# Performance work log

Measured on AMD Instinct MI355X. Metric: run time of the kernel, lower is better.

The kernel has to match this reference:

```python
import jax, jax.numpy as jnp
import numpy as np

B, L, N_APPS, EMB_DIM = 4096, 1024, 10, 2


def _linear_init(key, fan_in, fan_out):
    k1, k2 = jax.random.split(key)
    s = 1.0 / np.sqrt(fan_in)
    W = jax.random.uniform(k1, (fan_in, fan_out), minval=-s, maxval=s, dtype=jnp.float32)
    b = jax.random.uniform(k2, (fan_out,), minval=-s, maxval=s, dtype=jnp.float32)
    return W, b


def setup_inputs() -> dict:
    key = jax.random.key(0)
    ks = jax.random.split(key, 12)
    # features: row 0 carries integer-valued app ids (cast with .long() in torch)
    app_row = jax.random.randint(ks[0], (B, 1, L), 0, N_APPS).astype(jnp.float32)
    loads = jax.random.normal(ks[1], (B, 2, L), dtype=jnp.float32)
    features = jnp.concatenate([app_row, loads], axis=1)  # [B,3,L]
    x_app = jax.random.randint(ks[2], (B, 1), 0, N_APPS).astype(jnp.float32)
    x_load = jax.random.normal(ks[3], (B, 2), dtype=jnp.float32)
    x_features = jnp.concatenate([x_app, x_load], axis=1)  # [B,3]
    lengths = jax.random.randint(ks[4], (B,), 1, L + 1)  # dead in the math (see notes)
    emb = jax.random.normal(ks[5], (N_APPS, EMB_DIM), dtype=jnp.float32)
    fW1, fb1 = _linear_init(ks[6], EMB_DIM + 2, 50)
    fW2, fb2 = _linear_init(ks[7], 50, 25)
    fW3, fb3 = _linear_init(ks[8], 25, 5)
    rW1, rb1 = _linear_init(ks[9], 2 * 5 + EMB_DIM + 2, 50)
    rW2, rb2 = _linear_init(ks[10], 50, 25)
    rW3, rb3 = _linear_init(ks[11], 25, 1)
    return dict(x_features=x_features, features=features, lengths=lengths, emb=emb,
                fW1=fW1, fb1=fb1, fW2=fW2, fb2=fb2, fW3=fW3, fb3=fb3,
                rW1=rW1, rb1=rb1, rW2=rW2, rb2=rb2, rW3=rW3, rb3=rb3)


def _embed(table, idx):
    # nn.Embedding(max_norm=1.0): rows are renormalized to norm <= 1 at lookup
    e = table[idx]
    n = jnp.sqrt(jnp.sum(e * e, axis=-1, keepdims=True))
    return e * jnp.minimum(1.0, 1.0 / jnp.maximum(n, 1e-7))


def _mlp3(x, W1, b1, W2, b2, W3, b3):
    h = jax.nn.relu(x @ W1 + b1)
    h = jax.nn.relu(h @ W2 + b2)
    return h @ W3 + b3


def reference(x_features, features, lengths, emb,
              fW1, fb1, fW2, fb2, fW3, fb3,
              rW1, rb1, rW2, rb2, rW3, rb3):
    # NOTE: the torch forward slices xf[:, :xl] but then overwrites it with the
    # full-length rows, so `lengths` does not affect the math. Reproduced here.
    app_ids = features[:, 0, :].astype(jnp.int32)            # [B,L]
    loads = jnp.transpose(features[:, 1:, :], (0, 2, 1))     # [B,L,2]
    e = _embed(emb, app_ids)                                  # [B,L,2]
    h = jnp.concatenate([e, loads], axis=-1)                  # [B,L,4]
    h = _mlp3(h, fW1, fb1, fW2, fb2, fW3, fb3)                # [B,L,5]
    h_sum = jnp.sum(h, axis=1)                                # [B,5]
    h_max = jnp.max(h, axis=1)                                # [B,5]
    x_app = _embed(emb, x_features[:, 0].astype(jnp.int32))   # [B,2]
    x_f = jnp.concatenate([x_app, x_features[:, 1:]], axis=-1)  # [B,4]
    hh = jnp.concatenate([h_sum, h_max, x_f], axis=-1)        # [B,14]
    return _mlp3(hh, rW1, rb1, rW2, rb2, rW3, rb3)            # [B,1]
```

## Files before the change

### kernel.cpp

```cpp
#include <hip/hip_runtime.h>
#include <stdint.h>

#define BSZ 4096
#define LSEQ 1024

typedef _Float16 half8 __attribute__((ext_vector_type(8)));
typedef __fp16 fp16x2 __attribute__((ext_vector_type(2)));
typedef float f32x4 __attribute__((ext_vector_type(4)));

union S8 { int i[4]; half8 h; int4 q; };

__device__ __forceinline__ int pack_f16(float a, float b) {
    union { _Float16 h[2]; int i; } u;
    u.h[0] = (_Float16)a;
    u.h[1] = (_Float16)b;
    return u.i;
}
__device__ __forceinline__ int relu_pkrtz(float a, float b) {
    fp16x2 h = __builtin_amdgcn_cvt_pkrtz(a, b);
    h = __builtin_elementwise_max(h, (fp16x2)0.f);
    union { fp16x2 v; int i; } u;
    u.v = h;
    return u.i;
}
__device__ __forceinline__ void split_pair_f16(float a, float b, int& dh, int& dl) {
    _Float16 ah = (_Float16)a, bh = (_Float16)b;
    float al = a - (float)ah, bl = b - (float)bh;
    union { _Float16 h[2]; int i; } uh, ul;
    uh.h[0] = ah; uh.h[1] = bh;
    ul.h[0] = (_Float16)al; ul.h[1] = (_Float16)bl;
    dh = uh.i; dl = ul.i;
}
__device__ __forceinline__ f32x4 MFMA(half8 a, half8 b, f32x4 c) {
    return __builtin_amdgcn_mfma_f32_16x16x32_f16(a, b, c, 0, 0, 0);
}

#define WS_EMBH 5376
#define WS_EMBL 5392
#define WS_EMBR 5408

__global__ void sp_prep(const float* __restrict__ emb,
                        const float* __restrict__ fW1, const float* __restrict__ fb1,
                        const float* __restrict__ fW2, const float* __restrict__ fb2,
                        const float* __restrict__ fW3, const float* __restrict__ fb3,
                        int* __restrict__ ws)
{
    const int lane = threadIdx.x;
    const int L = lane & 15, g = lane >> 4;
    int4* wf = (int4*)ws;

    #pragma unroll
    for (int mt = 0; mt < 4; ++mt) {
        int j1 = ((mt >> 1) << 5) + ((L >> 2) << 3) + ((mt & 1) << 2) + (L & 3);
        float wv[4];
        _Float16 ah[4]; float alv[4];
        #pragma unroll
        for (int c = 0; c < 4; ++c) {
            wv[c] = (j1 < 50) ? fW1[c * 50 + j1] : 0.f;
            ah[c] = (_Float16)wv[c];
            alv[c] = wv[c] - (float)ah[c];
        }
        float bb = (j1 < 50) ? fb1[j1] : (j1 == 63 ? 1.f : 0.f);
        _Float16 bh = (_Float16)bb;
        float blv = bb - (float)bh;
        _Float16 v[8];
        #pragma unroll
        for (int e = 0; e < 8; ++e) {
            _Float16 x = (_Float16)0.f;
            if (g == 0) {
                if (e < 4) x = ah[e];
                else if (e < 6) x = ah[e - 4];
                else if (e == 6) x = bh;
            } else if (g == 1) {
                if (e < 4) x = (_Float16)alv[e];
                else if (e < 6) x = (_Float16)alv[e - 4];
                else if (e == 6) x = (_Float16)blv;
            }
            v[e] = x;
        }
        S8 F;
        #pragma unroll
        for (int d = 0; d < 4; ++d) {
            union { _Float16 h[2]; int i; } u;
            u.h[0] = v[2 * d]; u.h[1] = v[2 * d + 1];
            F.i[d] = u.i;
        }
        wf[mt * 64 + lane] = F.q;
    }

    #pragma unroll
    for (int kt = 0; kt < 2; ++kt) {
        #pragma unroll
        for (int mt2 = 0; mt2 < 2; ++mt2) {
            int j2 = ((L >> 2) << 3) + (mt2 << 2) + (L & 3);
            float w[8];
            #pragma unroll
            for (int r = 0; r < 8; ++r) {
                int j1v = kt * 32 + 8 * g + r;
                float wv = 0.f;
                if (j1v < 50)       wv = (j2 < 25) ? fW2[j1v * 25 + j2] : 0.f;
                else if (j1v == 63) wv = (j2 < 25) ? fb2[j2] : (j2 == 31 ? 1.f : 0.f);
                w[r] = wv;
            }
            S8 H, Lo;
            #pragma unroll
            for (int d = 0; d < 4; ++d) split_pair_f16(w[2*d], w[2*d+1], H.i[d], Lo.i[d]);
            wf[(4 + kt * 2 + mt2) * 64 + lane] = H.q;
            wf[(8 + kt * 2 + mt2) * 64 + lane] = Lo.q;
        }
    }

    {
        int m = L;
        float w[8];
        #pragma unroll
        for (int r = 0; r < 8; ++r) {
            int j2v = 8 * g + r;
            float wv = 0.f;
            if (j2v < 25)       wv = (m < 5) ? fW3[j2v * 5 + m] : 0.f;
            else if (j2v == 31) wv = (m < 5) ? fb3[m] : 0.f;
            w[r] = wv;
        }
        S8 H, Lo;
        #pragma unroll
        for (int d = 0; d < 4; ++d) split_pair_f16(w[2*d], w[2*d+1], H.i[d], Lo.i[d]);
        wf[12 * 64 + lane] = H.q;
        wf[13 * 64 + lane] = Lo.q;
    }

    if (lane < 10) {
        float a0 = emb[2 * lane], a1 = emb[2 * lane + 1];
        float n = sqrtf(a0 * a0 + a1 * a1);
        float s = fminf(1.f, 1.f / fmaxf(n, 1e-7f));
        float e0 = a0 * s, e1 = a1 * s;
        int dh, dl;
        split_pair_f16(e0, e1, dh, dl);
        ws[WS_EMBH + lane] = dh;
        ws[WS_EMBL + lane] = dl;
        ((float*)ws)[WS_EMBR + 2 * lane] = e0;
        ((float*)ws)[WS_EMBR + 2 * lane + 1] = e1;
    }
}

__global__ __launch_bounds__(256, 4) void sp_main(
    const float* __restrict__ x_features,
    const float* __restrict__ features,
    const int* __restrict__ ws,
    const float* __restrict__ rW1, const float* __restrict__ rb1,
    const float* __restrict__ rW2, const float* __restrict__ rb2,
    const float* __restrict__ rW3, const float* __restrict__ rb3,
    float* __restrict__ out)
{
    __shared__ int2 embhl[16];
    __shared__ float embr[20];
    __shared__ int4 bseq[LSEQ + 4];
    __shared__ float redS[4][5], redM[4][5];
    __shared__ float hhs[14];
    __shared__ float r1buf[50];

    const int t = threadIdx.x;
    const int b = blockIdx.x;
    const int lane = t & 63;
    const int wid = t >> 6;
    const int L = lane & 15;

    const int4* wf = (const int4*)ws;
    S8 A1[4], A2H[4], A2L[4], A3H, A3L;
    #pragma unroll
    for (int f = 0; f < 4; ++f)  A1[f].q  = wf[f * 64 + lane];
    #pragma unroll
    for (int f = 0; f < 4; ++f)  A2H[f].q = wf[(4 + f) * 64 + lane];
    #pragma unroll
    for (int f = 0; f < 4; ++f)  A2L[f].q = wf[(8 + f) * 64 + lane];
    A3H.q = wf[12 * 64 + lane];
    A3L.q = wf[13 * 64 + lane];

    if (t < 16) { embhl[t] = make_int2(ws[WS_EMBH + t], ws[WS_EMBL + t]); }
    if (t < 20) embr[t] = ((const float*)ws)[WS_EMBR + t];
    __syncthreads();

    const float* f0 = features + (size_t)b * (3 * LSEQ);
    #pragma unroll
    for (int j = 0; j < 4; ++j) {
        const int p = t + 256 * j;
        float av = f0[p];
        float bv = f0[LSEQ + p];
        float cv = f0[2 * LSEQ + p];
        int2 e = embhl[(int)av];
        bseq[p + j] = make_int4(e.x, pack_f16(bv, cv), e.y, 0x00003C00);
    }
    __syncthreads();

    float rs[4] = {0.f, 0.f, 0.f, 0.f};
    float rm[4] = {-3.4e38f, -3.4e38f, -3.4e38f, -3.4e38f};
    const f32x4 kzero = {0.f, 0.f, 0.f, 0.f};

    const int lbase = wid * 257 + L;

    #pragma unroll 2
    for (int it = 0; it < 8; ++it) {
        S8 B1a, B1b;
        B1a.q = bseq[lbase + it * 16];
        B1b.q = bseq[lbase + (it + 8) * 16];

        f32x4 h1a[4], h1b[4];
        #pragma unroll
        for (int mt = 0; mt < 4; ++mt) h1a[mt] = MFMA(A1[mt].h, B1a.h, kzero);
        #pragma unroll
        for (int mt = 0; mt < 4; ++mt) h1b[mt] = MFMA(A1[mt].h, B1b.h, kzero);

        S8 B20a, B21a;
        B20a.i[0] = relu_pkrtz(h1a[0][0], h1a[0][1]);
        B20a.i[1] = relu_pkrtz(h1a[0][2], h1a[0][3]);
        B20a.i[2] = relu_pkrtz(h1a[1][0], h1a[1][1]);
        B20a.i[3] = relu_pkrtz(h1a[1][2], h1a[1][3]);
        B21a.i[0] = relu_pkrtz(h1a[2][0], h1a[2][1]);
        B21a.i[1] = relu_pkrtz(h1a[2][2], h1a[2][3]);
        B21a.i[2] = relu_pkrtz(h1a[3][0], h1a[3][1]);
        B21a.i[3] = relu_pkrtz(h1a[3][2], h1a[3][3]);

        f32x4 h2a[2];
        #pragma unroll
        for (int mt2 = 0; mt2 < 2; ++mt2) {
            f32x4 acc = kzero;
            acc = MFMA(A2H[mt2].h,     B20a.h, acc);
            acc = MFMA(A2L[mt2].h,     B20a.h, acc);
            acc = MFMA(A2H[2 + mt2].h, B21a.h, acc);
            acc = MFMA(A2L[2 + mt2].h, B21a.h, acc);
            h2a[mt2] = acc;
        }

        S8 B20b, B21b;
        B20b.i[0] = relu_pkrtz(h1b[0][0], h1b[0][1]);
        B20b.i[1] = relu_pkrtz(h1b[0][2], h1b[0][3]);
        B20b.i[2] = relu_pkrtz(h1b[1][0], h1b[1][1]);
        B20b.i[3] = relu_pkrtz(h1b[1][2], h1b[1][3]);
        B21b.i[0] = relu_pkrtz(h1b[2][0], h1b[2][1]);
        B21b.i[1] = relu_pkrtz(h1b[2][2], h1b[2][3]);
        B21b.i[2] = relu_pkrtz(h1b[3][0], h1b[3][1]);
        B21b.i[3] = relu_pkrtz(h1b[3][2], h1b[3][3]);

        f32x4 h2b[2];
        #pragma unroll
        for (int mt2 = 0; mt2 < 2; ++mt2) {
            f32x4 acc = kzero;
            acc = MFMA(A2H[mt2].h,     B20b.h, acc);
            acc = MFMA(A2L[mt2].h,     B20b.h, acc);
            acc = MFMA(A2H[2 + mt2].h, B21b.h, acc);
            acc = MFMA(A2L[2 + mt2].h, B21b.h, acc);
            h2b[mt2] = acc;
        }

        S8 B3a;
        B3a.i[0] = relu_pkrtz(h2a[0][0], h2a[0][1]);
        B3a.i[1] = relu_pkrtz(h2a[0][2], h2a[0][3]);
        B3a.i[2] = relu_pkrtz(h2a[1][0], h2a[1][1]);
        B3a.i[3] = relu_pkrtz(h2a[1][2], h2a[1][3]);
        f32x4 h3a = MFMA(A3H.h, B3a.h, kzero);
        h3a = MFMA(A3L.h, B3a.h, h3a);

        S8 B3b;
        B3b.i[0] = relu_pkrtz(h2b[0][0], h2b[0][1]);
        B3b.i[1] = relu_pkrtz(h2b[0][2], h2b[0][3]);
        B3b.i[2] = relu_pkrtz(h2b[1][0], h2b[1][1]);
        B3b.i[3] = relu_pkrtz(h2b[1][2], h2b[1][3]);
        f32x4 h3b = MFMA(A3H.h, B3b.h, kzero);
        h3b = MFMA(A3L.h, B3b.h, h3b);

        #pragma unroll
        for (int r = 0; r < 4; ++r) {
            rs[r] += h3a[r] + h3b[r];
            rm[r] = fmaxf(rm[r], fmaxf(h3a[r], h3b[r]));
        }
    }

    #pragma unroll
    for (int off = 1; off <= 8; off <<= 1) {
        #pragma unroll
        for (int r = 0; r < 4; ++r) {
            rs[r] += __shfl_xor(rs[r], off);
            rm[r] = fmaxf(rm[r], __shfl_xor(rm[r], off));
        }
    }
    {
        const int kg = (lane >> 4);
        if (L == 0) {
            #pragma unroll
            for (int r = 0; r < 4; ++r) {
                int m = 4 * kg + r;
                if (m < 5) { redS[wid][m] = rs[r]; redM[wid][m] = rm[r]; }
            }
        }
    }
    __syncthreads();

    if (t < 5) {
        hhs[t] = (redS[0][t] + redS[1][t]) + (redS[2][t] + redS[3][t]);
    } else if (t < 10) {
        int m = t - 5;
        hhs[t] = fmaxf(fmaxf(redM[0][m], redM[1][m]), fmaxf(redM[2][m], redM[3][m]));
    } else if (t == 10) {
        int xa = (int)x_features[b * 3];
        hhs[10] = embr[2 * xa];
        hhs[11] = embr[2 * xa + 1];
        hhs[12] = x_features[b * 3 + 1];
        hhs[13] = x_features[b * 3 + 2];
    }
    __syncthreads();

    if (t < 50) {
        float acc = rb1[t];
        #pragma unroll
        for (int i = 0; i < 14; ++i) acc += hhs[i] * rW1[i * 50 + t];
        r1buf[t] = fmaxf(acc, 0.f);
    }
    __syncthreads();

    float oacc = 0.f;
    if (t < 25) {
        float acc = rb2[t];
        #pragma unroll
        for (int k = 0; k < 50; ++k) acc += r1buf[k] * rW2[k * 25 + t];
        oacc = fmaxf(acc, 0.f) * rW3[t];
    }
    if (t < 64) {
        #pragma unroll
        for (int off = 32; off > 0; off >>= 1) oacc += __shfl_down(oacc, off);
        if (t == 0) out[b] = oacc + rb3[0];
    }
}

extern "C" void kernel_launch(void* const* d_in, const int* in_sizes, int n_in,
                              void* d_out, int out_size, void* d_ws, size_t ws_size,
                              hipStream_t stream) {
    const float* x_features = (const float*)d_in[0];
    const float* features   = (const float*)d_in[1];
    const float* emb = (const float*)d_in[3];
    const float* fW1 = (const float*)d_in[4];
    const float* fb1 = (const float*)d_in[5];
    const float* fW2 = (const float*)d_in[6];
    const float* fb2 = (const float*)d_in[7];
    const float* fW3 = (const float*)d_in[8];
    const float* fb3 = (const float*)d_in[9];
    const float* rW1 = (const float*)d_in[10];
    const float* rb1 = (const float*)d_in[11];
    const float* rW2 = (const float*)d_in[12];
    const float* rb2 = (const float*)d_in[13];
    const float* rW3 = (const float*)d_in[14];
    const float* rb3 = (const float*)d_in[15];
    float* out = (float*)d_out;
    int* ws = (int*)d_ws;

    sp_prep<<<1, 64, 0, stream>>>(emb, fW1, fb1, fW2, fb2, fW3, fb3, ws);
    sp_main<<<BSZ, 256, 0, stream>>>(x_features, features, ws,
                                     rW1, rb1, rW2, rb2, rW3, rb3, out);
}
```

Baseline: 53.98 us.

## Process two batch rows per block with two waves per row

Each 256-thread block now handles two batch rows instead of one. Two waves share a row, each covering twice as many sequence positions, and the grid is halved. The aim is to amortize the per-block fixed costs (weight fragment loads into registers, embedding setup, barriers, and the serial regressor MLP tail) over more rows. In exchange LDS use per block roughly doubles, which may lower occupancy, and the tail regressor work now runs on two thread groups.

```diff
diff --git a/kernel.cpp b/kernel.cpp
--- a/kernel.cpp
+++ b/kernel.cpp
@@ -153,10 +153,10 @@
 {
     __shared__ int2 embhl[16];
     __shared__ float embr[20];
-    __shared__ int4 bseq[LSEQ + 4];
+    __shared__ int4 bseq[2][LSEQ + 4];
     __shared__ float redS[4][5], redM[4][5];
-    __shared__ float hhs[14];
-    __shared__ float r1buf[50];
+    __shared__ float hhs[2][14];
+    __shared__ float r1buf[2][50];
 
     const int t = threadIdx.x;
     const int b = blockIdx.x;
@@ -179,15 +179,19 @@
     if (t < 20) embr[t] = ((const float*)ws)[WS_EMBR + t];
     __syncthreads();
 
-    const float* f0 = features + (size_t)b * (3 * LSEQ);
-    #pragma unroll
-    for (int j = 0; j < 4; ++j) {
-        const int p = t + 256 * j;
-        float av = f0[p];
-        float bv = f0[LSEQ + p];
-        float cv = f0[2 * LSEQ + p];
-        int2 e = embhl[(int)av];
-        bseq[p + j] = make_int4(e.x, pack_f16(bv, cv), e.y, 0x00003C00);
+    const float* f0 = features + (size_t)(2 * b) * (3 * LSEQ);
+    #pragma unroll
+    for (int r = 0; r < 2; ++r) {
+        const float* fr = f0 + r * 3 * LSEQ;
+        #pragma unroll
+        for (int j = 0; j < 4; ++j) {
+            const int p = t + 256 * j;
+            float av = fr[p];
+            float bv = fr[LSEQ + p];
+            float cv = fr[2 * LSEQ + p];
+            int2 e = embhl[(int)av];
+            bseq[r][p + j] = make_int4(e.x, pack_f16(bv, cv), e.y, 0x00003C00);
+        }
     }
     __syncthreads();
 
@@ -195,13 +199,15 @@
     float rm[4] = {-3.4e38f, -3.4e38f, -3.4e38f, -3.4e38f};
     const f32x4 kzero = {0.f, 0.f, 0.f, 0.f};
 
-    const int lbase = wid * 257 + L;
+    const int wr = wid >> 1;
+    const int hw = wid & 1;
+    const int baseA = hw * 514 + L;
 
     #pragma unroll 2
-    for (int it = 0; it < 8; ++it) {
+    for (int it = 0; it < 16; ++it) {
         S8 B1a, B1b;
-        B1a.q = bseq[lbase + it * 16];
-        B1b.q = bseq[lbase + (it + 8) * 16];
+        B1a.q = bseq[wr][baseA + it * 16];
+        B1b.q = bseq[wr][baseA + it * 16 + 257];
 
         f32x4 h1a[4], h1b[4];
         #pragma unroll
@@ -295,24 +301,39 @@
     __syncthreads();
 
     if (t < 5) {
-        hhs[t] = (redS[0][t] + redS[1][t]) + (redS[2][t] + redS[3][t]);
+        hhs[0][t] = redS[0][t] + redS[1][t];
     } else if (t < 10) {
-        int m = t - 5;
-        hhs[t] = fmaxf(fmaxf(redM[0][m], redM[1][m]), fmaxf(redM[2][m], redM[3][m]));
+        hhs[0][t] = fmaxf(redM[0][t - 5], redM[1][t - 5]);
     } else if (t == 10) {
-        int xa = (int)x_features[b * 3];
-        hhs[10] = embr[2 * xa];
-        hhs[11] = embr[2 * xa + 1];
-        hhs[12] = x_features[b * 3 + 1];
-        hhs[13] = x_features[b * 3 + 2];
+        int xa = (int)x_features[6 * b];
+        hhs[0][10] = embr[2 * xa];
+        hhs[0][11] = embr[2 * xa + 1];
+        hhs[0][12] = x_features[6 * b + 1];
+        hhs[0][13] = x_features[6 * b + 2];
+    } else if (t >= 128 && t < 133) {
+        hhs[1][t - 128] = redS[2][t - 128] + redS[3][t - 128];
+    } else if (t >= 133 && t < 138) {
+        hhs[1][t - 128] = fmaxf(redM[2][t - 133], redM[3][t - 133]);
+    } else if (t == 138) {
+        int xa = (int)x_features[6 * b + 3];
+        hhs[1][10] = embr[2 * xa];
+        hhs[1][11] = embr[2 * xa + 1];
+        hhs[1][12] = x_features[6 * b + 4];
+        hhs[1][13] = x_features[6 * b + 5];
     }
     __syncthreads();
 
     if (t < 50) {
         float acc = rb1[t];
         #pragma unroll
-        for (int i = 0; i < 14; ++i) acc += hhs[i] * rW1[i * 50 + t];
-        r1buf[t] = fmaxf(acc, 0.f);
+        for (int i = 0; i < 14; ++i) acc += hhs[0][i] * rW1[i * 50 + t];
+        r1buf[0][t] = fmaxf(acc, 0.f);
+    } else if (t >= 128 && t < 178) {
+        int tt = t - 128;
+        float acc = rb1[tt];
+        #pragma unroll
+        for (int i = 0; i < 14; ++i) acc += hhs[1][i] * rW1[i * 50 + tt];
+        r1buf[1][tt] = fmaxf(acc, 0.f);
     }
     __syncthreads();
 
@@ -320,14 +341,21 @@
     if (t < 25) {
         float acc = rb2[t];
         #pragma unroll
-        for (int k = 0; k < 50; ++k) acc += r1buf[k] * rW2[k * 25 + t];
+        for (int k = 0; k < 50; ++k) acc += r1buf[0][k] * rW2[k * 25 + t];
         oacc = fmaxf(acc, 0.f) * rW3[t];
-    }
-    if (t < 64) {
+    } else if (t >= 128 && t < 153) {
+        int tt = t - 128;
+        float acc = rb2[tt];
+        #pragma unroll
+        for (int k = 0; k < 50; ++k) acc += r1buf[1][k] * rW2[k * 25 + tt];
+        oacc = fmaxf(acc, 0.f) * rW3[tt];
+    }
+    if (t < 64 || (t >= 128 && t < 192)) {
         #pragma unroll
         for (int off = 32; off > 0; off >>= 1) oacc += __shfl_down(oacc, off);
-        if (t == 0) out[b] = oacc + rb3[0];
-    }
+    }
+    if (t == 0)   out[2 * b]     = oacc + rb3[0];
+    if (t == 128) out[2 * b + 1] = oacc + rb3[0];
 }
 
 extern "C" void kernel_launch(void* const* d_in, const int* in_sizes, int n_in,
@@ -352,6 +380,6 @@
     int* ws = (int*)d_ws;
 
     sp_prep<<<1, 64, 0, stream>>>(emb, fW1, fb1, fW2, fb2, fW3, fb3, ws);
-    sp_main<<<BSZ, 256, 0, stream>>>(x_features, features, ws,
-                                     rW1, rb1, rW2, rb2, rW3, rb3, out);
-}
+    sp_main<<<BSZ / 2, 256, 0, stream>>>(x_features, features, ws,
+                                         rW1, rb1, rW2, rb2, rW3, rb3, out);
+}
```

Result: no change. 53.25 us (-1.4%).
